# Performance work log

Hardware: AMD Instinct MI355X
Metric: run time of the kernel (lower is better)

The kernel has to match this reference:

```python
import jax, jax.numpy as jnp
import numpy as np

OUT_H, OUT_W = 7, 7
SPATIAL_SCALE = 1.0


def setup_inputs() -> dict:
    key = jax.random.key(0)
    B, C, H, W = 4, 256, 64, 64
    N = 128
    features = jax.random.normal(key, (B, C, H, W), dtype=jnp.float32)
    rng = np.random.default_rng(0)
    bidx = rng.integers(0, B, N)
    x1 = rng.integers(0, W - 8, N)
    y1 = rng.integers(0, H - 8, N)
    x2 = np.minimum(x1 + rng.integers(4, 48, N), W - 1)
    y2 = np.minimum(y1 + rng.integers(4, 48, N), H - 1)
    rois = jnp.asarray(np.stack([bidx, x1, y1, x2, y2], axis=1), dtype=jnp.int32)
    return {"features": features, "rois": rois}


def _bin_bounds(n_bins, bin_sz, roi_sz):
    # h_start = int(h*bin_h); h_end = int((h+1)*bin_h); then clamp as in torch code
    bins = jnp.arange(n_bins)
    start = jnp.floor(bins[None, :] * bin_sz[:, None]).astype(jnp.int32)
    end = jnp.floor((bins[None, :] + 1) * bin_sz[:, None]).astype(jnp.int32)
    start = jnp.minimum(start, roi_sz[:, None] - 1)
    end = jnp.minimum(end, roi_sz[:, None])
    return start, end  # [N, n_bins]


def _roi_pool(features, rois):
    B, C, H, W = features.shape
    b = rois[:, 0]
    coords = (rois[:, 1:5].astype(jnp.float32) * SPATIAL_SCALE).astype(jnp.int32)
    x1, y1, x2, y2 = coords[:, 0], coords[:, 1], coords[:, 2], coords[:, 3]
    roi_h = y2 - y1 + 1  # inclusive slice y1:y2+1
    roi_w = x2 - x1 + 1
    bin_h = roi_h.astype(jnp.float32) / OUT_H
    bin_w = roi_w.astype(jnp.float32) / OUT_W

    hs, he = _bin_bounds(OUT_H, bin_h, roi_h)  # [N, OUT_H]
    ws, we = _bin_bounds(OUT_W, bin_w, roi_w)  # [N, OUT_W]
    valid = (he > hs)[:, :, None] & (we > ws)[:, None, :]  # [N, OUT_H, OUT_W]

    yy = jnp.arange(H)
    xx = jnp.arange(W)
    # absolute-coordinate bin masks (factorized along H and W)
    mask_h = (yy[None, None, :] >= (y1[:, None] + hs)[:, :, None]) & (
        yy[None, None, :] < (y1[:, None] + he)[:, :, None])  # [N, OUT_H, H]
    mask_w = (xx[None, None, :] >= (x1[:, None] + ws)[:, :, None]) & (
        xx[None, None, :] < (x1[:, None] + we)[:, :, None])  # [N, OUT_W, W]

    feat = features[b]  # [N, C, H, W] gather per ROI
    NEG = jnp.array(-jnp.inf, features.dtype)
    # reduce H per output row bin (OUT_H is small, fixed)
    rows = [jnp.where(mask_h[:, i, None, :, None], feat, NEG).max(axis=2)
            for i in range(OUT_H)]  # each [N, C, W]
    rowmax = jnp.stack(rows, axis=1)  # [N, OUT_H, C, W]
    cols = [jnp.where(mask_w[:, j, None, None, :], rowmax, NEG).max(axis=3)
            for j in range(OUT_W)]  # each [N, OUT_H, C]
    pooled = jnp.stack(cols, axis=3)  # [N, OUT_H, C, OUT_W]
    pooled = jnp.transpose(pooled, (0, 2, 1, 3))  # [N, C, OUT_H, OUT_W]
    # empty bins (h_end<=h_start or w_end<=w_start) stay zero, as in the torch code
    return jnp.where(valid[:, None, :, :], pooled, jnp.zeros((), features.dtype))


def reference(features, rois):
    return _roi_pool(features, rois)
```

## Files before the change

kernel.cpp:

```cpp
#include <hip/hip_runtime.h>
#include <math.h>

#define OUT_H 7
#define OUT_W 7
#define NBINS 49
#define RFL(x) __builtin_amdgcn_readfirstlane(x)

__global__ __launch_bounds__(256) void roipool_v13(
    const float* __restrict__ feat, const int* __restrict__ rois,
    float* __restrict__ out)
{
    constexpr int C = 256, H = 64, W = 64, HW = H * W;
    __shared__ float racc_lds[4][OUT_H][65];

    const int bx   = blockIdx.x;
    const int n    = bx >> 6;
    const int cg   = bx & 63;
    const int tid  = threadIdx.x;
    const int lane = tid & 63;
    const int wave = RFL(tid >> 6);
    const int c    = cg * 4 + wave;

    const int* r = rois + n * 5;
    const int b  = RFL(r[0]);
    const int x1 = RFL(r[1]);
    const int y1 = RFL(r[2]);
    const int roi_w = RFL(r[3]) - x1 + 1;
    const int roi_h = RFL(r[4]) - y1 + 1;

    const float* plane = feat + (size_t)(b * C + c) * HW;

    int hb[OUT_H + 1];
#pragma unroll
    for (int k = 0; k <= OUT_H; ++k) hb[k] = RFL((k * roi_h) / OUT_H);

    float racc[OUT_H];
#pragma unroll
    for (int ph = 0; ph < OUT_H; ++ph) {
        const int rb = (y1 + hb[ph]) * W;
        int rl = (y1 + hb[ph + 1] - 1) * W;
        rl = rl > rb ? rl : rb;
        int r1 = rb + 1 * W; r1 = r1 < rl ? r1 : rl;
        int r2 = rb + 2 * W; r2 = r2 < rl ? r2 : rl;
        int r3 = rb + 3 * W; r3 = r3 < rl ? r3 : rl;
        const float v0 = plane[rb + lane];
        const float v1 = plane[r1 + lane];
        const float v2 = plane[r2 + lane];
        const float v3 = plane[r3 + lane];
        racc[ph] = fmaxf(fmaxf(v0, v1), fmaxf(v2, v3));
    }
#pragma unroll
    for (int ph = 0; ph < OUT_H; ++ph) {
        const int h = hb[ph + 1] - hb[ph];
        if (h > 4) {
            const int rb = (y1 + hb[ph]) * W;
            const int rl = (y1 + hb[ph + 1] - 1) * W;
            int r4 = rb + 4 * W; r4 = r4 < rl ? r4 : rl;
            int r5 = rb + 5 * W; r5 = r5 < rl ? r5 : rl;
            int r6 = rb + 6 * W; r6 = r6 < rl ? r6 : rl;
            const float v4 = plane[r4 + lane];
            const float v5 = plane[r5 + lane];
            const float v6 = plane[r6 + lane];
            racc[ph] = fmaxf(racc[ph], fmaxf(v4, fmaxf(v5, v6)));
        }
    }

#pragma unroll
    for (int ph = 0; ph < OUT_H; ++ph) racc_lds[wave][ph][lane] = racc[ph];

    if (lane < NBINS) {
        const int ph = lane / OUT_W;
        const int pw = lane - ph * OUT_W;

        const int hsL = (ph * roi_h) / OUT_H;
        const int heL = ((ph + 1) * roi_h) / OUT_H;
        const int ws  = (pw * roi_w) / OUT_W;
        const int we  = ((pw + 1) * roi_w) / OUT_W;

        const int xs = x1 + ws;
        int xl = x1 + we - 1;
        xl = xl > xs ? xl : xs;

        float g[8];
#pragma unroll
        for (int j = 0; j < 8; ++j) {
            int x = xs + j;
            x = x < xl ? x : xl;
            g[j] = racc_lds[wave][ph][x];
        }
        float m = fmaxf(fmaxf(fmaxf(g[0], g[1]), fmaxf(g[2], g[3])),
                        fmaxf(fmaxf(g[4], g[5]), fmaxf(g[6], g[7])));

        const bool valid = (heL > hsL) && (we > ws);
        out[(size_t)(n * C + c) * NBINS + lane] = valid ? m : 0.0f;
    }
}

extern "C" void kernel_launch(void* const* d_in, const int* in_sizes, int n_in,
                              void* d_out, int out_size, void* d_ws, size_t ws_size,
                              hipStream_t stream) {
    const float* feat = (const float*)d_in[0];
    const int*   rois = (const int*)d_in[1];
    float*       out  = (float*)d_out;

    const int N = in_sizes[1] / 5;
    const int n_blocks = N * 64;

    roipool_v13<<<n_blocks, 256, 0, stream>>>(feat, rois, out);
}
```

Measured before the change: 75.96 us.

## Load two image rows per wave with float2 and merge halves in LDS

Each wave now reads two adjacent rows at once with float2 loads: the low 32 lanes cover one row and the high 32 lanes cover the next. This halves the number of load instructions needed per row bin. The two half-row partial maxima are written to a doubled LDS slab and combined during the column reduction. Single-row bins need special masking with -inf, including the edge case at the last row, which adds index logic and LDS traffic.

```diff
diff --git a/kernel.cpp b/kernel.cpp
--- a/kernel.cpp
+++ b/kernel.cpp
@@ -6,12 +6,12 @@
 #define NBINS 49
 #define RFL(x) __builtin_amdgcn_readfirstlane(x)
 
-__global__ __launch_bounds__(256) void roipool_v13(
+__global__ __launch_bounds__(256) void roipool_v16(
     const float* __restrict__ feat, const int* __restrict__ rois,
     float* __restrict__ out)
 {
     constexpr int C = 256, H = 64, W = 64, HW = H * W;
-    __shared__ float racc_lds[4][OUT_H][65];
+    __shared__ float slab[4][2][OUT_H][W];
 
     const int bx   = blockIdx.x;
     const int n    = bx >> 6;
@@ -29,44 +29,70 @@
     const int roi_h = RFL(r[4]) - y1 + 1;
 
     const float* plane = feat + (size_t)(b * C + c) * HW;
+    const bool hi_half = (lane >= 32);
 
     int hb[OUT_H + 1];
 #pragma unroll
     for (int k = 0; k <= OUT_H; ++k) hb[k] = RFL((k * roi_h) / OUT_H);
 
-    float racc[OUT_H];
+    float2 racc[OUT_H];
+
 #pragma unroll
     for (int ph = 0; ph < OUT_H; ++ph) {
-        const int rb = (y1 + hb[ph]) * W;
-        int rl = (y1 + hb[ph + 1] - 1) * W;
-        rl = rl > rb ? rl : rb;
-        int r1 = rb + 1 * W; r1 = r1 < rl ? r1 : rl;
-        int r2 = rb + 2 * W; r2 = r2 < rl ? r2 : rl;
-        int r3 = rb + 3 * W; r3 = r3 < rl ? r3 : rl;
-        const float v0 = plane[rb + lane];
-        const float v1 = plane[r1 + lane];
-        const float v2 = plane[r2 + lane];
-        const float v3 = plane[r3 + lane];
-        racc[ph] = fmaxf(fmaxf(v0, v1), fmaxf(v2, v3));
+        const int h  = hb[ph + 1] - hb[ph];
+        const int yb = y1 + hb[ph];
+        int s0 = yb;
+        if (h <= 1) s0 = yb <= 62 ? yb : 62;
+        const bool hi_bad = (h == 1) && (yb <= 62);
+        const bool lo_bad = (h == 1) && (yb == 63);
+        const float2 v = ((const float2*)(plane + s0 * W))[lane];
+        const bool kill = hi_half ? hi_bad : lo_bad;
+        racc[ph].x = kill ? -INFINITY : v.x;
+        racc[ph].y = kill ? -INFINITY : v.y;
+    }
+#pragma unroll
+    for (int ph = 0; ph < OUT_H; ++ph) {
+        const int h = hb[ph + 1] - hb[ph];
+        if (h > 2) {
+            const int yb = y1 + hb[ph];
+            const int yl = yb + h - 1;
+            int s = yb + 2; s = s < yl - 1 ? s : yl - 1;
+            const float2 v = ((const float2*)(plane + s * W))[lane];
+            racc[ph].x = fmaxf(racc[ph].x, v.x);
+            racc[ph].y = fmaxf(racc[ph].y, v.y);
+        }
     }
 #pragma unroll
     for (int ph = 0; ph < OUT_H; ++ph) {
         const int h = hb[ph + 1] - hb[ph];
         if (h > 4) {
-            const int rb = (y1 + hb[ph]) * W;
-            const int rl = (y1 + hb[ph + 1] - 1) * W;
-            int r4 = rb + 4 * W; r4 = r4 < rl ? r4 : rl;
-            int r5 = rb + 5 * W; r5 = r5 < rl ? r5 : rl;
-            int r6 = rb + 6 * W; r6 = r6 < rl ? r6 : rl;
-            const float v4 = plane[r4 + lane];
-            const float v5 = plane[r5 + lane];
-            const float v6 = plane[r6 + lane];
-            racc[ph] = fmaxf(racc[ph], fmaxf(v4, fmaxf(v5, v6)));
+            const int yb = y1 + hb[ph];
+            const int yl = yb + h - 1;
+            int s = yb + 4; s = s < yl - 1 ? s : yl - 1;
+            const float2 v = ((const float2*)(plane + s * W))[lane];
+            racc[ph].x = fmaxf(racc[ph].x, v.x);
+            racc[ph].y = fmaxf(racc[ph].y, v.y);
+        }
+    }
+#pragma unroll
+    for (int ph = 0; ph < OUT_H; ++ph) {
+        const int h = hb[ph + 1] - hb[ph];
+        if (h > 6) {
+            const int yb = y1 + hb[ph];
+            const int yl = yb + h - 1;
+            int s = yb + 6; s = s < yl - 1 ? s : yl - 1;
+            const float2 v = ((const float2*)(plane + s * W))[lane];
+            racc[ph].x = fmaxf(racc[ph].x, v.x);
+            racc[ph].y = fmaxf(racc[ph].y, v.y);
         }
     }
 
+    const int half = lane >> 5;
+    const int lx2  = (lane & 31) * 2;
 #pragma unroll
-    for (int ph = 0; ph < OUT_H; ++ph) racc_lds[wave][ph][lane] = racc[ph];
+    for (int ph = 0; ph < OUT_H; ++ph) {
+        *(float2*)&slab[wave][half][ph][lx2] = racc[ph];
+    }
 
     if (lane < NBINS) {
         const int ph = lane / OUT_W;
@@ -86,7 +112,7 @@
         for (int j = 0; j < 8; ++j) {
             int x = xs + j;
             x = x < xl ? x : xl;
-            g[j] = racc_lds[wave][ph][x];
+            g[j] = fmaxf(slab[wave][0][ph][x], slab[wave][1][ph][x]);
         }
         float m = fmaxf(fmaxf(fmaxf(g[0], g[1]), fmaxf(g[2], g[3])),
                         fmaxf(fmaxf(g[4], g[5]), fmaxf(g[6], g[7])));
@@ -106,5 +132,5 @@
     const int N = in_sizes[1] / 5;
     const int n_blocks = N * 64;
 
-    roipool_v13<<<n_blocks, 256, 0, stream>>>(feat, rois, out);
+    roipool_v16<<<n_blocks, 256, 0, stream>>>(feat, rois, out);
 }
```

Measured after the change: 81.64 us. 1.07x slower.
